# Optimization experiments

Measured on AMD Instinct MI355X. Metric: run time of the kernel, lower is better.

The kernel has to match this reference:

```python
import jax, jax.numpy as jnp
import numpy as np

B, C, H, W = 16, 256, 128, 128
NF = 8
GN_GROUPS = 8
EPS = 1e-5


def setup_inputs() -> dict:
    key = jax.random.key(0)
    k0, k1, k2, k3 = jax.random.split(key, 4)
    return {
        "x": jax.random.normal(k0, (B, C, H, W), dtype=jnp.float32),
        # learned params
        "filter_bank": jax.random.normal(k1, (NF, 1, 7, 7), dtype=jnp.float32) * 0.02,
        "sel_w": jax.random.normal(k2, (NF, C), dtype=jnp.float32) / np.float32(np.sqrt(C)),
        "sel_b": jnp.zeros((NF,), dtype=jnp.float32),
        "proj_w": jax.random.normal(k3, (C, C, 1, 1), dtype=jnp.float32) / np.float32(np.sqrt(C)),
        "proj_b": jnp.zeros((C,), dtype=jnp.float32),
        "gn_gamma": jnp.ones((C,), dtype=jnp.float32),
        "gn_beta": jnp.zeros((C,), dtype=jnp.float32),
    }


def reference(x, filter_bank, sel_w, sel_b, proj_w, proj_b, gn_gamma, gn_beta):
    b, c, h, w = x.shape
    # filter selector: GAP -> Linear -> softmax
    pooled = x.mean(axis=(2, 3))                       # [B, C]
    weights = jax.nn.softmax(pooled @ sel_w.T + sel_b, axis=-1)  # [B, NF]
    # softmax-weighted mix of the 7x7 filter bank -> one filter per sample
    combined = jnp.einsum('bn,nhw->bhw', weights, filter_bank[:, 0])  # [B, 7, 7]
    # per-sample depthwise conv: each sample's filter applied to all C channels
    kern = jnp.repeat(combined[:, None], c, axis=0)    # [B*C, 1, 7, 7] (sample-major, matches reshape)
    filtered = jax.lax.conv_general_dilated(
        x.reshape(1, b * c, h, w), kern,
        window_strides=(1, 1), padding=((3, 3), (3, 3)),
        feature_group_count=b * c,
        dimension_numbers=('NCHW', 'OIHW', 'NCHW'),
    ).reshape(b, c, h, w)
    # output projection: 1x1 conv
    y = jnp.einsum('bchw,oc->bohw', filtered, proj_w[:, :, 0, 0]) + proj_b[None, :, None, None]
    # GroupNorm(8, C) with affine
    yg = y.reshape(b, GN_GROUPS, c // GN_GROUPS, h, w)
    mean = yg.mean(axis=(2, 3, 4), keepdims=True)
    var = yg.var(axis=(2, 3, 4), keepdims=True)
    yn = ((yg - mean) * jax.lax.rsqrt(var + EPS)).reshape(b, c, h, w)
    yn = yn * gn_gamma[None, :, None, None] + gn_beta[None, :, None, None]
    # exact GELU (torch default) + residual
    return jax.nn.gelu(yn, approximate=False) + x
```

## Files before the change

kernel.cpp:

```cpp
#include <hip/hip_runtime.h>
#include <math.h>

#define BB 16
#define CC 256
#define HH 128
#define WW 128
#define HWSZ 16384
#define NF 8
#define EPSV 1e-5f

typedef __attribute__((ext_vector_type(8))) short short8;
typedef __attribute__((ext_vector_type(4))) float f32x4;

static __device__ __forceinline__ unsigned short f2bf(float f) {
  unsigned int u = __float_as_uint(f);
  u += 0x7fffu + ((u >> 16) & 1u);
  return (unsigned short)(u >> 16);
}

static __device__ __forceinline__ float bf2f(unsigned int h) {
  return __uint_as_float(h << 16);
}

static __device__ __forceinline__ void gload_lds16(const unsigned short* g,
                                                   unsigned short* l) {
  __builtin_amdgcn_global_load_lds(
      (const __attribute__((address_space(1))) void*)(size_t)g,
      (__attribute__((address_space(3))) void*)(unsigned)(size_t)l, 16, 0, 0);
}

__global__ __launch_bounds__(256) void pool_pack_kernel(
    const float* __restrict__ x, const float* __restrict__ pw,
    float* __restrict__ pooled, unsigned short* __restrict__ ap) {
  int blk = blockIdx.x;
  int tid = threadIdx.x;
  if (blk >= BB * CC) {
    int idx = (blk - BB * CC) * 256 + tid;
    int e = idx & 7;
    int lane = (idx >> 3) & 63;
    int kb = (idx >> 9) & 7;
    int mb = idx >> 12;
    int o = mb * 16 + (lane & 15);
    int c = kb * 32 + (lane >> 4) * 8 + e;
    ap[idx] = f2bf(pw[o * 256 + c]);
    return;
  }
  const float4* xp = (const float4*)(x + (size_t)blk * HWSZ);
  float s = 0.f;
#pragma unroll
  for (int i = 0; i < 16; ++i) {
    float4 v = xp[tid + i * 256];
    s += v.x + v.y + v.z + v.w;
  }
#pragma unroll
  for (int off = 32; off > 0; off >>= 1) s += __shfl_down(s, off, 64);
  __shared__ float ls[4];
  if ((tid & 63) == 0) ls[tid >> 6] = s;
  __syncthreads();
  if (tid == 0) pooled[blk] = (ls[0] + ls[1] + ls[2] + ls[3]) * (1.0f / 16384.0f);
}

__global__ __launch_bounds__(256) void selector_kernel(
    const float* __restrict__ pooled, const float* __restrict__ sel_w,
    const float* __restrict__ sel_b, const float* __restrict__ fbank,
    float* __restrict__ combined) {
  int tid = threadIdx.x;
  __shared__ float lg[BB][NF];
  __shared__ float wsm[BB][NF];
  if (tid < BB * NF) {
    int b = tid >> 3, n = tid & 7;
    const float* p = pooled + b * CC;
    const float* w = sel_w + n * CC;
    float d = sel_b[n];
    for (int c = 0; c < CC; c += 4) {
      d += p[c] * w[c] + p[c + 1] * w[c + 1] + p[c + 2] * w[c + 2] + p[c + 3] * w[c + 3];
    }
    lg[b][n] = d;
  }
  __syncthreads();
  if (tid < BB) {
    int b = tid;
    float m = lg[b][0];
#pragma unroll
    for (int n = 1; n < NF; ++n) m = fmaxf(m, lg[b][n]);
    float e[NF];
    float s = 0.f;
#pragma unroll
    for (int n = 0; n < NF; ++n) { e[n] = expf(lg[b][n] - m); s += e[n]; }
    float inv = 1.0f / s;
#pragma unroll
    for (int n = 0; n < NF; ++n) wsm[b][n] = e[n] * inv;
  }
  __syncthreads();
  for (int i = tid; i < BB * 49; i += 256) {
    int b = i / 49, j = i % 49;
    float acc = 0.f;
#pragma unroll
    for (int n = 0; n < NF; ++n) acc += wsm[b][n] * fbank[n * 49 + j];
    combined[b * 64 + j] = acc;
  }
}

#define TR 64
__global__ __launch_bounds__(256) void dwconv_kernel(
    const float* __restrict__ x, const float* __restrict__ combined,
    unsigned short* __restrict__ fbp) {
  int plane = blockIdx.x;
  int rt = blockIdx.y;
  int b = plane >> 8;
  int r0 = rt * TR;
  int tid = threadIdx.x;

  __shared__ float xs[TR + 6][136];

  float kf[49];
  {
    const float* cb = combined + b * 64;
#pragma unroll
    for (int i = 0; i < 49; ++i) kf[i] = cb[i];
  }

  const size_t pbase = (size_t)plane * HWSZ;
  for (int idx = tid; idx < (TR + 6) * 34; idx += 256) {
    int row = idx / 34;
    int seg = idx % 34;
    int r = r0 - 3 + row;
    int c = seg * 4 - 4;
    float4 v = make_float4(0.f, 0.f, 0.f, 0.f);
    if (r >= 0 && r < HH && c >= 0 && c < WW) {
      v = *(const float4*)(x + pbase + (size_t)r * WW + c);
    }
    *(float4*)&xs[row][seg * 4] = v;
  }
  __syncthreads();

  int cg = tid & 31;
  int rg = tid >> 5;
  float acc[8][4] = {};

#pragma unroll
  for (int ri = 0; ri < 14; ++ri) {
    int lrow = 8 * rg + ri;
    float xr[12];
#pragma unroll
    for (int s = 0; s < 3; ++s)
      *(float4*)&xr[4 * s] = *(const float4*)&xs[lrow][cg * 4 + 4 * s];
#pragma unroll
    for (int orr = 0; orr < 8; ++orr) {
      int dy = ri - orr;
      if (dy < 0 || dy > 6) continue;
#pragma unroll
      for (int oc = 0; oc < 4; ++oc) {
#pragma unroll
        for (int dx = 0; dx < 7; ++dx) {
          acc[orr][oc] += xr[oc + dx + 1] * kf[dy * 7 + dx];
        }
      }
    }
  }

#pragma unroll
  for (int orr = 0; orr < 8; ++orr) {
    ushort4 sv;
    sv.x = f2bf(acc[orr][0]);
    sv.y = f2bf(acc[orr][1]);
    sv.z = f2bf(acc[orr][2]);
    sv.w = f2bf(acc[orr][3]);
    *(ushort4*)(fbp + pbase + (size_t)(r0 + 8 * rg + orr) * WW + 4 * cg) = sv;
  }
}

#define SWZ(p) ((((p) >> 1) ^ ((p) >> 4)) & 3)

__global__ __launch_bounds__(512, 2) void gemm_kernel(
    const unsigned short* __restrict__ fb, const unsigned short* __restrict__ ap,
    const float* __restrict__ proj_b, unsigned short* __restrict__ yb,
    float* __restrict__ part) {
  int bid = blockIdx.x;
  int bs = bid >> 7;
  int pt = bid & 127;
  int p0 = pt * 128;
  int tid = threadIdx.x;
  int lane = tid & 63;
  int wave = tid >> 6;
  int wm = wave >> 1;
  int wn = wave & 1;

  __shared__ __align__(16) unsigned short A_lds[3][8192];
  __shared__ __align__(16) unsigned short B_lds[3][4096];

  const unsigned short* asrc0 =
      ap + (size_t)(tid >> 6) * 4096 + (size_t)(tid & 63) * 8;
  unsigned short* adst = &A_lds[0][0] + (size_t)tid * 8;

  int cp = tid >> 5;
  int pq = tid & 31;
  const unsigned short* bsrc0 =
      fb + ((size_t)bs * CC + 2 * cp) * HWSZ + p0 + 4 * pq;

  uint2 bregs[4][2];

#define STAGE_A(kb, buf)                                                      \
  do {                                                                        \
    gload_lds16(asrc0 + (size_t)(kb) * 512, adst + (size_t)(buf) * 8192);     \
    gload_lds16(asrc0 + 32768 + (size_t)(kb) * 512,                           \
                adst + (size_t)(buf) * 8192 + 4096);                          \
  } while (0)
#define LOAD_B(kb, slot)                                                      \
  do {                                                                        \
    const unsigned short* s_ = bsrc0 + (size_t)(kb) * 32 * HWSZ;              \
    bregs[slot][0] = *(const uint2*)s_;                                       \
    bregs[slot][1] = *(const uint2*)(s_ + HWSZ);                              \
  } while (0)
#define WRITE_B(slot, buf)                                                    \
  do {                                                                        \
    unsigned int w0_[2] = {bregs[slot][0].x, bregs[slot][0].y};               \
    unsigned int w1_[2] = {bregs[slot][1].x, bregs[slot][1].y};               \
    _Pragma("unroll")                                                         \
    for (int j_ = 0; j_ < 4; ++j_) {                                          \
      int p_ = 4 * pq + j_;                                                   \
      int cc_ = (2 * cp) ^ (SWZ(p_) << 3);                                    \
      unsigned int lo_ = (w0_[j_ >> 1] >> ((j_ & 1) * 16)) & 0xffffu;         \
      unsigned int hi_ = (w1_[j_ >> 1] >> ((j_ & 1) * 16)) & 0xffffu;         \
      *(unsigned int*)&B_lds[buf][p_ * 32 + cc_] = lo_ | (hi_ << 16);         \
    }                                                                         \
  } while (0)

  STAGE_A(0, 0);
  LOAD_B(0, 0);
  STAGE_A(1, 1);
  LOAD_B(1, 1);
  LOAD_B(2, 2);

  f32x4 acc[4][4];
#pragma unroll
  for (int mb = 0; mb < 4; ++mb)
#pragma unroll
    for (int nb = 0; nb < 4; ++nb) acc[mb][nb] = (f32x4){0.f, 0.f, 0.f, 0.f};

  int aofs[4];
#pragma unroll
  for (int mb = 0; mb < 4; ++mb) aofs[mb] = ((wm * 4 + mb) * 64 + lane) * 8;
  int bofs[4];
#pragma unroll
  for (int nb = 0; nb < 4; ++nb) {
    int pp = wn * 64 + nb * 16 + (lane & 15);
    bofs[nb] = pp * 32 + (((lane >> 4) * 8) ^ (SWZ(pp) << 3));
  }

  asm volatile("s_waitcnt vmcnt(6)" ::: "memory");
  WRITE_B(0, 0);
  asm volatile("s_waitcnt lgkmcnt(0)" ::: "memory");
  __builtin_amdgcn_s_barrier();

#pragma unroll
  for (int kb = 0; kb < 8; ++kb) {
    const int cur = kb % 3;
    const int n1 = (kb + 1) % 3;
    if (kb < 6) STAGE_A(kb + 2, (kb + 2) % 3);
    if (kb < 5) LOAD_B(kb + 3, (kb + 3) & 3);
    if (kb < 6) __builtin_amdgcn_sched_barrier(0);
    short8 af[4], bfr[4];
#pragma unroll
    for (int mb = 0; mb < 4; ++mb)
      af[mb] = *(const short8*)(&A_lds[cur][0] + aofs[mb]);
#pragma unroll
    for (int nb = 0; nb < 4; ++nb)
      bfr[nb] = *(const short8*)(&B_lds[cur][0] + bofs[nb]);
    if (kb <= 4) {
      asm volatile("s_waitcnt vmcnt(6)" ::: "memory");
      WRITE_B((kb + 1) & 3, n1);
    } else if (kb == 5) {
      asm volatile("s_waitcnt vmcnt(4)" ::: "memory");
      WRITE_B((kb + 1) & 3, n1);
    } else if (kb == 6) {
      asm volatile("s_waitcnt vmcnt(0)" ::: "memory");
      WRITE_B((kb + 1) & 3, n1);
    }
    asm volatile("s_waitcnt lgkmcnt(0)" ::: "memory");
    __builtin_amdgcn_sched_barrier(0);
    __builtin_amdgcn_s_setprio(1);
#pragma unroll
    for (int mb = 0; mb < 4; ++mb)
#pragma unroll
      for (int nb = 0; nb < 4; ++nb)
        acc[mb][nb] = __builtin_amdgcn_mfma_f32_16x16x32_bf16(
            af[mb], bfr[nb], acc[mb][nb], 0, 0, 0);
    __builtin_amdgcn_s_setprio(0);
    if (kb < 7) __builtin_amdgcn_s_barrier();
  }

  float psum[2] = {0.f, 0.f}, psq[2] = {0.f, 0.f};
  int orl = (lane >> 4) * 4;
  int pl = lane & 15;
  const size_t ybase = (size_t)bs * CC * HWSZ + p0 + wn * 64;
  int obase = wm * 64;
#pragma unroll
  for (int mb = 0; mb < 4; ++mb) {
    int gi = mb >> 1;
#pragma unroll
    for (int r = 0; r < 4; ++r) {
      int o = obase + mb * 16 + orl + r;
      float pb = proj_b[o];
      unsigned short* yrow = yb + ybase + (size_t)o * HWSZ + pl;
#pragma unroll
      for (int nb = 0; nb < 4; ++nb) {
        float v = acc[mb][nb][r] + pb;
        yrow[nb * 16] = f2bf(v);
        psum[gi] += v;
        psq[gi] += v * v;
      }
    }
  }
#pragma unroll
  for (int off = 32; off > 0; off >>= 1) {
#pragma unroll
    for (int k = 0; k < 2; ++k) {
      psum[k] += __shfl_down(psum[k], off, 64);
      psq[k] += __shfl_down(psq[k], off, 64);
    }
  }
  if (lane == 0) {
#pragma unroll
    for (int k = 0; k < 2; ++k) {
      int bg = bs * 8 + wm * 2 + k;
      part[(size_t)bg * 256 + pt * 2 + wn] = psum[k];
      part[32768 + (size_t)bg * 256 + pt * 2 + wn] = psq[k];
    }
  }
#undef STAGE_A
#undef LOAD_B
#undef WRITE_B
}

__global__ __launch_bounds__(256) void out_kernel(
    const float* __restrict__ x, const unsigned short* __restrict__ yb,
    const float* __restrict__ part, const float* __restrict__ gamma,
    const float* __restrict__ beta, float* __restrict__ out) {
  int plane = blockIdx.x;
  int b = plane >> 8, c = plane & 255, g = c >> 5;
  int bg = b * 8 + g;
  int t = threadIdx.x;

  float s = part[(size_t)bg * 256 + t];
  float q = part[32768 + (size_t)bg * 256 + t];
#pragma unroll
  for (int off = 32; off > 0; off >>= 1) {
    s += __shfl_down(s, off, 64);
    q += __shfl_down(q, off, 64);
  }
  __shared__ float ls[8];
  if ((t & 63) == 0) { ls[t >> 6] = s; ls[4 + (t >> 6)] = q; }
  __syncthreads();
  float tsum = ls[0] + ls[1] + ls[2] + ls[3];
  float tsq = ls[4] + ls[5] + ls[6] + ls[7];

  const float inv_n = 1.0f / (32.0f * (float)HWSZ);
  float mean = tsum * inv_n;
  float var = tsq * inv_n - mean * mean;
  float rstd = rsqrtf(var + EPSV);
  float scale = gamma[c] * rstd;
  float shift = beta[c] - mean * scale;

  const size_t base = (size_t)plane * HWSZ;
  for (int i = t; i < HWSZ / 8; i += 256) {
    uint4 yv = *(const uint4*)(yb + base + 8 * (size_t)i);
    float4 x0 = *(const float4*)(x + base + 8 * (size_t)i);
    float4 x1 = *(const float4*)(x + base + 8 * (size_t)i + 4);
    unsigned int yw[4] = {yv.x, yv.y, yv.z, yv.w};
    float r[8];
    float xr[8] = {x0.x, x0.y, x0.z, x0.w, x1.x, x1.y, x1.z, x1.w};
#pragma unroll
    for (int k = 0; k < 8; ++k) {
      unsigned int h = (yw[k >> 1] >> ((k & 1) * 16)) & 0xffffu;
      float tv = bf2f(h) * scale + shift;
      float ge = 0.5f * tv * (1.0f + erff(tv * 0.70710678118654752f));
      r[k] = ge + xr[k];
    }
    *(float4*)(out + base + 8 * (size_t)i) = make_float4(r[0], r[1], r[2], r[3]);
    *(float4*)(out + base + 8 * (size_t)i + 4) = make_float4(r[4], r[5], r[6], r[7]);
  }
}

extern "C" void kernel_launch(void* const* d_in, const int* in_sizes, int n_in,
                              void* d_out, int out_size, void* d_ws, size_t ws_size,
                              hipStream_t stream) {
  const float* x      = (const float*)d_in[0];
  const float* fbank  = (const float*)d_in[1];
  const float* sel_w  = (const float*)d_in[2];
  const float* sel_b  = (const float*)d_in[3];
  const float* proj_w = (const float*)d_in[4];
  const float* proj_b = (const float*)d_in[5];
  const float* gamma  = (const float*)d_in[6];
  const float* beta   = (const float*)d_in[7];
  float* out = (float*)d_out;

  unsigned short* fb  = (unsigned short*)d_ws;
  unsigned short* yb  = fb + (size_t)BB * CC * HWSZ;
  unsigned short* apk = yb + (size_t)BB * CC * HWSZ;
  float* pooled   = (float*)(apk + 65536);
  float* combined = pooled + BB * CC;
  float* part     = combined + BB * 64;

  hipLaunchKernelGGL(pool_pack_kernel, dim3(BB * CC + 256), dim3(256), 0, stream,
                     x, proj_w, pooled, apk);
  hipLaunchKernelGGL(selector_kernel, dim3(1), dim3(256), 0, stream,
                     pooled, sel_w, sel_b, fbank, combined);
  hipLaunchKernelGGL(dwconv_kernel, dim3(BB * CC, HH / TR), dim3(256), 0, stream,
                     x, combined, fb);
  hipLaunchKernelGGL(gemm_kernel, dim3(BB * 128), dim3(512), 0, stream,
                     fb, apk, proj_b, yb, part);
  hipLaunchKernelGGL(out_kernel, dim3(BB * CC), dim3(256), 0, stream,
                     x, yb, part, gamma, beta, out);
}
```

Before: 405.1 us.

## Fuse selector into depthwise conv and stage GEMM output through LDS

Removes the single-block selector kernel: each dwconv block now recomputes the softmax filter weights and the combined 7x7 filter for its sample from pooled values, overlapping that with its LDS tile load. This drops one launch and a serial single-CU stage, at the cost of redundant small compute in every block. The GEMM epilogue now writes bf16 results into LDS reused from the operand buffers, then stores them to global as 16-byte vectors per row instead of scattered 2-byte stores, which adds a barrier and LDS traffic.

```diff
diff --git a/kernel.cpp b/kernel.cpp
--- a/kernel.cpp
+++ b/kernel.cpp
@@ -60,51 +60,11 @@
   if (tid == 0) pooled[blk] = (ls[0] + ls[1] + ls[2] + ls[3]) * (1.0f / 16384.0f);
 }
 
-__global__ __launch_bounds__(256) void selector_kernel(
-    const float* __restrict__ pooled, const float* __restrict__ sel_w,
-    const float* __restrict__ sel_b, const float* __restrict__ fbank,
-    float* __restrict__ combined) {
-  int tid = threadIdx.x;
-  __shared__ float lg[BB][NF];
-  __shared__ float wsm[BB][NF];
-  if (tid < BB * NF) {
-    int b = tid >> 3, n = tid & 7;
-    const float* p = pooled + b * CC;
-    const float* w = sel_w + n * CC;
-    float d = sel_b[n];
-    for (int c = 0; c < CC; c += 4) {
-      d += p[c] * w[c] + p[c + 1] * w[c + 1] + p[c + 2] * w[c + 2] + p[c + 3] * w[c + 3];
-    }
-    lg[b][n] = d;
-  }
-  __syncthreads();
-  if (tid < BB) {
-    int b = tid;
-    float m = lg[b][0];
-#pragma unroll
-    for (int n = 1; n < NF; ++n) m = fmaxf(m, lg[b][n]);
-    float e[NF];
-    float s = 0.f;
-#pragma unroll
-    for (int n = 0; n < NF; ++n) { e[n] = expf(lg[b][n] - m); s += e[n]; }
-    float inv = 1.0f / s;
-#pragma unroll
-    for (int n = 0; n < NF; ++n) wsm[b][n] = e[n] * inv;
-  }
-  __syncthreads();
-  for (int i = tid; i < BB * 49; i += 256) {
-    int b = i / 49, j = i % 49;
-    float acc = 0.f;
-#pragma unroll
-    for (int n = 0; n < NF; ++n) acc += wsm[b][n] * fbank[n * 49 + j];
-    combined[b * 64 + j] = acc;
-  }
-}
-
 #define TR 64
 __global__ __launch_bounds__(256) void dwconv_kernel(
-    const float* __restrict__ x, const float* __restrict__ combined,
-    unsigned short* __restrict__ fbp) {
+    const float* __restrict__ x, const float* __restrict__ pooled,
+    const float* __restrict__ sel_w, const float* __restrict__ sel_b,
+    const float* __restrict__ fbank, unsigned short* __restrict__ fbp) {
   int plane = blockIdx.x;
   int rt = blockIdx.y;
   int b = plane >> 8;
@@ -112,13 +72,8 @@
   int tid = threadIdx.x;
 
   __shared__ float xs[TR + 6][136];
-
-  float kf[49];
-  {
-    const float* cb = combined + b * 64;
-#pragma unroll
-    for (int i = 0; i < 49; ++i) kf[i] = cb[i];
-  }
+  __shared__ float wsm[NF];
+  __shared__ float cmb[64];
 
   const size_t pbase = (size_t)plane * HWSZ;
   for (int idx = tid; idx < (TR + 6) * 34; idx += 256) {
@@ -132,7 +87,44 @@
     }
     *(float4*)&xs[row][seg * 4] = v;
   }
+
+  if (tid < 64) {
+    int n = tid >> 3, ck = tid & 7;
+    const float* p = pooled + b * CC + ck * 32;
+    const float* w = sel_w + n * CC + ck * 32;
+    float d = 0.f;
+#pragma unroll
+    for (int i = 0; i < 32; ++i) d += p[i] * w[i];
+    d += __shfl_down(d, 4, 8);
+    d += __shfl_down(d, 2, 8);
+    d += __shfl_down(d, 1, 8);
+    if (ck == 0) wsm[n] = d + sel_b[n];
+  }
   __syncthreads();
+  if (tid == 0) {
+    float m = wsm[0];
+#pragma unroll
+    for (int n = 1; n < NF; ++n) m = fmaxf(m, wsm[n]);
+    float e[NF];
+    float s = 0.f;
+#pragma unroll
+    for (int n = 0; n < NF; ++n) { e[n] = expf(wsm[n] - m); s += e[n]; }
+    float inv = 1.0f / s;
+#pragma unroll
+    for (int n = 0; n < NF; ++n) wsm[n] = e[n] * inv;
+  }
+  __syncthreads();
+  if (tid < 49) {
+    float a = 0.f;
+#pragma unroll
+    for (int n = 0; n < NF; ++n) a += wsm[n] * fbank[n * 49 + tid];
+    cmb[tid] = a;
+  }
+  __syncthreads();
+
+  float kf[49];
+#pragma unroll
+  for (int i = 0; i < 49; ++i) kf[i] = cmb[i];
 
   int cg = tid & 31;
   int rg = tid >> 5;
@@ -186,8 +178,9 @@
   int wm = wave >> 1;
   int wn = wave & 1;
 
-  __shared__ __align__(16) unsigned short A_lds[3][8192];
-  __shared__ __align__(16) unsigned short B_lds[3][4096];
+  __shared__ __align__(16) unsigned char smem[73728];
+  unsigned short (*A_lds)[8192] = (unsigned short (*)[8192])smem;
+  unsigned short (*B_lds)[4096] = (unsigned short (*)[4096])(smem + 49152);
 
   const unsigned short* asrc0 =
       ap + (size_t)(tid >> 6) * 4096 + (size_t)(tid & 63) * 8;
@@ -290,28 +283,37 @@
     if (kb < 7) __builtin_amdgcn_s_barrier();
   }
 
+  __builtin_amdgcn_s_barrier();
+
+  unsigned short* yt = (unsigned short*)smem + (size_t)wave * 4608;
   float psum[2] = {0.f, 0.f}, psq[2] = {0.f, 0.f};
   int orl = (lane >> 4) * 4;
   int pl = lane & 15;
-  const size_t ybase = (size_t)bs * CC * HWSZ + p0 + wn * 64;
-  int obase = wm * 64;
 #pragma unroll
   for (int mb = 0; mb < 4; ++mb) {
     int gi = mb >> 1;
 #pragma unroll
     for (int r = 0; r < 4; ++r) {
-      int o = obase + mb * 16 + orl + r;
-      float pb = proj_b[o];
-      unsigned short* yrow = yb + ybase + (size_t)o * HWSZ + pl;
+      int ol = mb * 16 + orl + r;
+      float pb = proj_b[wm * 64 + ol];
 #pragma unroll
       for (int nb = 0; nb < 4; ++nb) {
         float v = acc[mb][nb][r] + pb;
-        yrow[nb * 16] = f2bf(v);
+        yt[ol * 72 + pl + nb * 16] = f2bf(v);
         psum[gi] += v;
         psq[gi] += v * v;
       }
     }
   }
+  const size_t ybase = (size_t)bs * CC * HWSZ + p0 + wn * 64;
+#pragma unroll
+  for (int k = 0; k < 8; ++k) {
+    int idx = k * 64 + lane;
+    int ol = idx >> 3, ch = idx & 7;
+    uint4 v = *(const uint4*)(yt + ol * 72 + ch * 8);
+    *(uint4*)(yb + ybase + (size_t)(wm * 64 + ol) * HWSZ + ch * 8) = v;
+  }
+
 #pragma unroll
   for (int off = 32; off > 0; off >>= 1) {
 #pragma unroll
@@ -399,15 +401,12 @@
   unsigned short* yb  = fb + (size_t)BB * CC * HWSZ;
   unsigned short* apk = yb + (size_t)BB * CC * HWSZ;
   float* pooled   = (float*)(apk + 65536);
-  float* combined = pooled + BB * CC;
-  float* part     = combined + BB * 64;
+  float* part     = pooled + BB * CC;
 
   hipLaunchKernelGGL(pool_pack_kernel, dim3(BB * CC + 256), dim3(256), 0, stream,
                      x, proj_w, pooled, apk);
-  hipLaunchKernelGGL(selector_kernel, dim3(1), dim3(256), 0, stream,
-                     pooled, sel_w, sel_b, fbank, combined);
   hipLaunchKernelGGL(dwconv_kernel, dim3(BB * CC, HH / TR), dim3(256), 0, stream,
-                     x, combined, fb);
+                     x, pooled, sel_w, sel_b, fbank, fb);
   hipLaunchKernelGGL(gemm_kernel, dim3(BB * 128), dim3(512), 0, stream,
                      fb, apk, proj_b, yb, part);
   hipLaunchKernelGGL(out_kernel, dim3(BB * CC), dim3(256), 0, stream,
```

New measurement: 457.7 us. 13.0% more time.

## Stage bf16 copy of x for dwconv and coalesce GEMM output stores via LDS

Applied to the files above, without the earlier changes.

The pooling pass now also writes a bf16 copy of x into the output buffer, used as scratch, and the depthwise conv reads that half-size copy instead of fp32 x. The intent is to cut conv read traffic at the cost of an extra write pass and reduced input precision. Separately, the GEMM epilogue stages bf16 results in reused LDS so that each wave writes full 16-byte row chunks instead of scattered 2-byte stores. That adds a barrier and LDS round-trip per tile.

```diff
diff --git a/kernel.cpp b/kernel.cpp
--- a/kernel.cpp
+++ b/kernel.cpp
@@ -31,7 +31,8 @@
 
 __global__ __launch_bounds__(256) void pool_pack_kernel(
     const float* __restrict__ x, const float* __restrict__ pw,
-    float* __restrict__ pooled, unsigned short* __restrict__ ap) {
+    float* __restrict__ pooled, unsigned short* __restrict__ ap,
+    unsigned short* __restrict__ xb) {
   int blk = blockIdx.x;
   int tid = threadIdx.x;
   if (blk >= BB * CC) {
@@ -46,11 +47,18 @@
     return;
   }
   const float4* xp = (const float4*)(x + (size_t)blk * HWSZ);
+  ushort4* xbp = (ushort4*)(xb + (size_t)blk * HWSZ);
   float s = 0.f;
 #pragma unroll
   for (int i = 0; i < 16; ++i) {
     float4 v = xp[tid + i * 256];
     s += v.x + v.y + v.z + v.w;
+    ushort4 bv;
+    bv.x = f2bf(v.x);
+    bv.y = f2bf(v.y);
+    bv.z = f2bf(v.z);
+    bv.w = f2bf(v.w);
+    xbp[tid + i * 256] = bv;
   }
 #pragma unroll
   for (int off = 32; off > 0; off >>= 1) s += __shfl_down(s, off, 64);
@@ -103,7 +111,7 @@
 
 #define TR 64
 __global__ __launch_bounds__(256) void dwconv_kernel(
-    const float* __restrict__ x, const float* __restrict__ combined,
+    const unsigned short* __restrict__ xb, const float* __restrict__ combined,
     unsigned short* __restrict__ fbp) {
   int plane = blockIdx.x;
   int rt = blockIdx.y;
@@ -128,7 +136,11 @@
     int c = seg * 4 - 4;
     float4 v = make_float4(0.f, 0.f, 0.f, 0.f);
     if (r >= 0 && r < HH && c >= 0 && c < WW) {
-      v = *(const float4*)(x + pbase + (size_t)r * WW + c);
+      uint2 u = *(const uint2*)(xb + pbase + (size_t)r * WW + c);
+      v.x = __uint_as_float(u.x << 16);
+      v.y = __uint_as_float(u.x & 0xffff0000u);
+      v.z = __uint_as_float(u.y << 16);
+      v.w = __uint_as_float(u.y & 0xffff0000u);
     }
     *(float4*)&xs[row][seg * 4] = v;
   }
@@ -186,8 +198,9 @@
   int wm = wave >> 1;
   int wn = wave & 1;
 
-  __shared__ __align__(16) unsigned short A_lds[3][8192];
-  __shared__ __align__(16) unsigned short B_lds[3][4096];
+  __shared__ __align__(16) unsigned char smem[73728];
+  unsigned short (*A_lds)[8192] = (unsigned short (*)[8192])smem;
+  unsigned short (*B_lds)[4096] = (unsigned short (*)[4096])(smem + 49152);
 
   const unsigned short* asrc0 =
       ap + (size_t)(tid >> 6) * 4096 + (size_t)(tid & 63) * 8;
@@ -290,28 +303,37 @@
     if (kb < 7) __builtin_amdgcn_s_barrier();
   }
 
+  __builtin_amdgcn_s_barrier();
+
+  unsigned short* yt = (unsigned short*)smem + (size_t)wave * 4608;
   float psum[2] = {0.f, 0.f}, psq[2] = {0.f, 0.f};
   int orl = (lane >> 4) * 4;
   int pl = lane & 15;
-  const size_t ybase = (size_t)bs * CC * HWSZ + p0 + wn * 64;
-  int obase = wm * 64;
 #pragma unroll
   for (int mb = 0; mb < 4; ++mb) {
     int gi = mb >> 1;
 #pragma unroll
     for (int r = 0; r < 4; ++r) {
-      int o = obase + mb * 16 + orl + r;
-      float pb = proj_b[o];
-      unsigned short* yrow = yb + ybase + (size_t)o * HWSZ + pl;
+      int ol = mb * 16 + orl + r;
+      float pb = proj_b[wm * 64 + ol];
 #pragma unroll
       for (int nb = 0; nb < 4; ++nb) {
         float v = acc[mb][nb][r] + pb;
-        yrow[nb * 16] = f2bf(v);
+        yt[ol * 72 + pl + nb * 16] = f2bf(v);
         psum[gi] += v;
         psq[gi] += v * v;
       }
     }
   }
+  const size_t ybase = (size_t)bs * CC * HWSZ + p0 + wn * 64;
+#pragma unroll
+  for (int k = 0; k < 8; ++k) {
+    int idx = k * 64 + lane;
+    int ol = idx >> 3, ch = idx & 7;
+    uint4 v = *(const uint4*)(yt + ol * 72 + ch * 8);
+    *(uint4*)(yb + ybase + (size_t)(wm * 64 + ol) * HWSZ + ch * 8) = v;
+  }
+
 #pragma unroll
   for (int off = 32; off > 0; off >>= 1) {
 #pragma unroll
@@ -401,13 +423,14 @@
   float* pooled   = (float*)(apk + 65536);
   float* combined = pooled + BB * CC;
   float* part     = combined + BB * 64;
+  unsigned short* xb = (unsigned short*)d_out;
 
   hipLaunchKernelGGL(pool_pack_kernel, dim3(BB * CC + 256), dim3(256), 0, stream,
-                     x, proj_w, pooled, apk);
+                     x, proj_w, pooled, apk, xb);
   hipLaunchKernelGGL(selector_kernel, dim3(1), dim3(256), 0, stream,
                      pooled, sel_w, sel_b, fbank, combined);
   hipLaunchKernelGGL(dwconv_kernel, dim3(BB * CC, HH / TR), dim3(256), 0, stream,
-                     x, combined, fb);
+                     xb, combined, fb);
   hipLaunchKernelGGL(gemm_kernel, dim3(BB * 128), dim3(512), 0, stream,
                      fb, apk, proj_b, yb, part);
   hipLaunchKernelGGL(out_kernel, dim3(BB * CC), dim3(256), 0, stream,
```

New measurement: 430.3 us. 1.06x slower.
